# Optimization experiments

Measured on AMD Instinct MI355X. Metric: run time of the kernel, lower is better.

The kernel has to match this reference:

```python
import jax, jax.numpy as jnp
import numpy as np

# Per-level grid spatial shapes: ceil([T,H,W]/grid_size/2**i) + 1 with
# video (T,H,W) = (120,1080,1920), grid_size=8, n_levels=2.
GRID_SHAPES = [jnp.array([16.0, 136.0, 241.0], dtype=jnp.float32),
               jnp.array([9.0, 69.0, 121.0], dtype=jnp.float32)]
EMB_DIM = 16
N_PTS = 1_000_000

# 8 binary corner offsets, MSB-first bit order (matches f'{i:03b}').
OFFSETS = jnp.array([[(i >> 2) & 1, (i >> 1) & 1, i & 1] for i in range(8)],
                    dtype=jnp.float32)  # [8,3]


def setup_inputs() -> dict:
    key = jax.random.key(0)
    k0, k1, k2 = jax.random.split(key, 3)
    inputs = jax.random.uniform(k0, (N_PTS, 3), dtype=jnp.float32)
    emb0 = jax.random.normal(k1, (16, 136, 241, EMB_DIM), dtype=jnp.float32)
    emb1 = jax.random.normal(k2, (9, 69, 121, EMB_DIM), dtype=jnp.float32)
    return {"inputs": inputs, "emb0": emb0, "emb1": emb1}


def _encode_level(inputs, emb, gshape):
    # inputs: [N,3] in [0,1]; emb: [T,H,W,D]; gshape: [3] float grid shape
    coords = inputs * (gshape - 1.0)                         # [N,3]
    corner = jnp.floor(coords[:, None, :] + OFFSETS)         # [N,8,3]
    corner = jnp.clip(corner, 0.0, gshape - 1.0)             # [N,8,3]
    idx = corner.astype(jnp.int32)
    values = emb[idx[..., 0], idx[..., 1], idx[..., 2]]      # [N,8,D] gather
    weights = jnp.prod(1.0 - jnp.abs(corner - coords[:, None, :]),
                       axis=-1, keepdims=True)               # [N,8,1]
    return jnp.sum(weights * values, axis=-2)                # [N,D]


def reference(inputs, emb0, emb1):
    out0 = _encode_level(inputs, emb0, GRID_SHAPES[0])
    out1 = _encode_level(inputs, emb1, GRID_SHAPES[1])
    return jnp.concatenate([out0, out1], axis=-1)            # [N, 2*D]
```

## Files before the change

kernel.cpp:

```cpp
#include <hip/hip_runtime.h>


typedef float floatx4 __attribute__((ext_vector_type(4)));

#define KXB 8
#define KYB 17
#define KZB 31
#define NBINS (KXB * KYB * KZB)
#define NSUB 4
#define CAPS 104
#define CAP_TOT (NSUB * CAPS)
#define CNT_DWORDS (NSUB * NBINS + 1)

#define L0X 3
#define L0Y 9
#define L0Z 9
#define L0CELLS (L0X * L0Y * L0Z)
#define CSTR 20

__device__ __forceinline__ int point_key(float px, float py, float pz) {
    int ix = (int)(px * 15.0f);  ix = min(max(ix, 0), 15);
    int iy = (int)(py * 135.0f); iy = min(max(iy, 0), 135);
    int iz = (int)(pz * 240.0f); iz = min(max(iz, 0), 240);
    return ((ix >> 1) * KYB + (iy >> 3)) * KZB + (iz >> 3);
}

__device__ __forceinline__ void load4pts(const float* __restrict__ pts, int i4,
                                         float px[4], float py[4], float pz[4]) {
    const floatx4* v = (const floatx4*)(pts + (size_t)i4 * 3);
    const floatx4 a = v[0], b = v[1], c = v[2];
    px[0] = a.x; py[0] = a.y; pz[0] = a.z;
    px[1] = a.w; py[1] = b.x; pz[1] = b.y;
    px[2] = b.z; py[2] = b.w; pz[2] = c.x;
    px[3] = c.y; py[3] = c.z; pz[3] = c.w;
}

__global__ __launch_bounds__(256)
void k_zero(unsigned* __restrict__ cnt) {
    const int i = blockIdx.x * blockDim.x + threadIdx.x;
    if (i < CNT_DWORDS) cnt[i] = 0u;
}

__global__ __launch_bounds__(256)
void k_bin(const float* __restrict__ pts, int n,
           unsigned* __restrict__ cnt, unsigned* __restrict__ ovfc,
           unsigned* __restrict__ slots, unsigned* __restrict__ ovf) {
    const int i4 = (blockIdx.x * blockDim.x + threadIdx.x) * 4;
    if (i4 >= n) return;
    if (i4 + 3 < n) {
        float px[4], py[4], pz[4];
        load4pts(pts, i4, px, py, pz);
        int k[4];
#pragma unroll
        for (int j = 0; j < 4; ++j) k[j] = point_key(px[j], py[j], pz[j]);
        unsigned pos[4];
#pragma unroll
        for (int j = 0; j < 4; ++j)
            pos[j] = atomicAdd(&cnt[j * NBINS + k[j]], 1u);
#pragma unroll
        for (int j = 0; j < 4; ++j) {
            if (pos[j] < CAPS)
                slots[(size_t)k[j] * CAP_TOT + j * CAPS + pos[j]] = (unsigned)(i4 + j);
            else
                ovf[atomicAdd(ovfc, 1u)] = (unsigned)(i4 + j);
        }
    } else {
        for (int j = 0; j < 4 && i4 + j < n; ++j) {
            const size_t b = (size_t)(i4 + j) * 3;
            const int k = point_key(pts[b], pts[b+1], pts[b+2]);
            const unsigned pos = atomicAdd(&cnt[j * NBINS + k], 1u);
            if (pos < CAPS) slots[(size_t)k * CAP_TOT + j * CAPS + pos] = (unsigned)(i4 + j);
            else            ovf[atomicAdd(ovfc, 1u)] = (unsigned)(i4 + j);
        }
    }
}

__device__ __forceinline__ void setup_lds(float cx, float cy, float cz,
                                          int xb, int yb, int zb, int d,
                                          int* __restrict__ off,
                                          float* __restrict__ w) {
    float gx[2] = { floorf(cx), floorf(cx + 1.0f) };
    float gy[2] = { floorf(cy), floorf(cy + 1.0f) };
    float gz[2] = { floorf(cz), floorf(cz + 1.0f) };
    float wx[2], wy[2], wz[2];
    int   xo[2], yo[2], zo[2];
#pragma unroll
    for (int b = 0; b < 2; ++b) {
        gx[b] = fminf(fmaxf(gx[b], 0.0f), 15.0f);
        gy[b] = fminf(fmaxf(gy[b], 0.0f), 135.0f);
        gz[b] = fminf(fmaxf(gz[b], 0.0f), 240.0f);
        wx[b] = 1.0f - fabsf(gx[b] - cx);
        wy[b] = 1.0f - fabsf(gy[b] - cy);
        wz[b] = 1.0f - fabsf(gz[b] - cz);
        xo[b] = min((int)gx[b] - xb, L0X - 1) * (L0Y * L0Z * CSTR);
        yo[b] = min((int)gy[b] - yb, L0Y - 1) * (L0Z * CSTR);
        zo[b] = min((int)gz[b] - zb, L0Z - 1) * CSTR + d;
    }
    float wyz[4];
    int   yzo[4];
#pragma unroll
    for (int j = 0; j < 2; ++j)
#pragma unroll
        for (int k = 0; k < 2; ++k) {
            wyz[2 * j + k] = wy[j] * wz[k];
            yzo[2 * j + k] = yo[j] + zo[k];
        }
#pragma unroll
    for (int c = 0; c < 8; ++c) {
        const int i = (c >> 2) & 1, jk = c & 3;
        w[c]   = wx[i] * wyz[jk];
        off[c] = xo[i] + yzo[jk];
    }
}

__device__ __forceinline__ void setup_glb(float cx, float cy, float cz,
                                          float tm1, float hm1, float wm1,
                                          int sh, int sw, int d,
                                          int* __restrict__ off,
                                          float* __restrict__ w) {
    float gx[2] = { floorf(cx), floorf(cx + 1.0f) };
    float gy[2] = { floorf(cy), floorf(cy + 1.0f) };
    float gz[2] = { floorf(cz), floorf(cz + 1.0f) };
    float wx[2], wy[2], wz[2];
    int   xo[2], yo[2], zo[2];
#pragma unroll
    for (int b = 0; b < 2; ++b) {
        gx[b] = fminf(fmaxf(gx[b], 0.0f), tm1);
        gy[b] = fminf(fmaxf(gy[b], 0.0f), hm1);
        gz[b] = fminf(fmaxf(gz[b], 0.0f), wm1);
        wx[b] = 1.0f - fabsf(gx[b] - cx);
        wy[b] = 1.0f - fabsf(gy[b] - cy);
        wz[b] = 1.0f - fabsf(gz[b] - cz);
        xo[b] = (int)gx[b] * sh;
        yo[b] = (int)gy[b] * sw;
        zo[b] = (int)gz[b] * 16 + d;
    }
    float wyz[4];
    int   yzo[4];
#pragma unroll
    for (int j = 0; j < 2; ++j)
#pragma unroll
        for (int k = 0; k < 2; ++k) {
            wyz[2 * j + k] = wy[j] * wz[k];
            yzo[2 * j + k] = yo[j] + zo[k];
        }
#pragma unroll
    for (int c = 0; c < 8; ++c) {
        const int i = (c >> 2) & 1, jk = c & 3;
        w[c]   = wx[i] * wyz[jk];
        off[c] = xo[i] + yzo[jk];
    }
}

__device__ __forceinline__ void encode_glb_quad(int p, int lane4,
                                                const float* __restrict__ pts,
                                                const float* __restrict__ emb0,
                                                const float* __restrict__ emb1,
                                                float* __restrict__ out) {
    const size_t b = (size_t)p * 3;
    const float px = pts[b], py = pts[b + 1], pz = pts[b + 2];
    int   o0[8], o1[8];
    float w0[8], w1[8];
    setup_glb(px * 15.0f, py * 135.0f, pz * 240.0f, 15.0f, 135.0f, 240.0f,
              136 * 241 * 16, 241 * 16, lane4, o0, w0);
    setup_glb(px * 8.0f, py * 68.0f, pz * 120.0f, 8.0f, 68.0f, 120.0f,
              69 * 121 * 16, 121 * 16, lane4, o1, w1);
    floatx4 a0 = {0,0,0,0}, a1 = {0,0,0,0};
#pragma unroll
    for (int c = 0; c < 8; ++c) a0 += w0[c] * *(const floatx4*)(emb0 + o0[c]);
#pragma unroll
    for (int c = 0; c < 8; ++c) a1 += w1[c] * *(const floatx4*)(emb1 + o1[c]);
    float* row = out + (size_t)p * 32 + lane4;
    __builtin_nontemporal_store(a0, (floatx4*)row);
    __builtin_nontemporal_store(a1, (floatx4*)(row + 16));
}

__global__ __launch_bounds__(256, 4)
void k_main_bins(const unsigned* __restrict__ slots,
                 const unsigned* __restrict__ cnt,
                 const unsigned* __restrict__ ovfc,
                 const unsigned* __restrict__ ovf,
                 const float* __restrict__ pts,
                 const float* __restrict__ emb0,
                 const float* __restrict__ emb1,
                 float* __restrict__ out) {
    const int bin = (blockIdx.x & 7) * 527 + (blockIdx.x >> 3);
    const unsigned n0 = min(cnt[bin],             (unsigned)CAPS);
    const unsigned n1 = min(cnt[NBINS + bin],     (unsigned)CAPS);
    const unsigned n2 = min(cnt[2 * NBINS + bin], (unsigned)CAPS);
    const unsigned n3 = min(cnt[3 * NBINS + bin], (unsigned)CAPS);
    const unsigned c0 = n0, c1 = c0 + n1, c2 = c1 + n2, nt = c2 + n3;

    __shared__ float lds0[L0CELLS * CSTR];

    const int tid = threadIdx.x;
    const int d = (tid & 3) * 4;

    if (nt != 0) {
        const int bz = bin % KZB;
        const int t1 = bin / KZB;
        const int by = t1 % KYB;
        const int bx = t1 / KYB;

        const int x0 = bx * 2, y0 = by * 8, z0 = bz * 8;

        for (int idx = tid; idx < L0CELLS * 4; idx += 256) {
            const int cell = idx >> 2, q = (idx & 3) * 4;
            const int lz = cell % L0Z;
            const int t = cell / L0Z;
            const int ly = t % L0Y, lx = t / L0Y;
            const int gx = min(x0 + lx, 15), gy = min(y0 + ly, 135), gz = min(z0 + lz, 240);
            const floatx4 v = *(const floatx4*)(emb0 + ((size_t)(gx * 136 + gy) * 241 + gz) * 16 + q);
            *(floatx4*)(lds0 + cell * CSTR + q) = v;
        }
        __syncthreads();

        const int quad = tid >> 2;
        const size_t sbase = (size_t)bin * CAP_TOT;

        auto slot_of = [&](unsigned t) -> unsigned {
            const unsigned seg = (t >= c0) + (t >= c1) + (t >= c2);
            const unsigned base = (seg == 0) ? 0u : ((seg == 1) ? c0 : ((seg == 2) ? c1 : c2));
            return (unsigned)(sbase + seg * CAPS + (t - base));
        };

        unsigned tA = quad, tB = quad + 64;
        int origA = (int)slots[slot_of(min(tA, nt - 1))];
        int origB = (int)slots[slot_of(min(tB, nt - 1))];
        size_t pbA = (size_t)origA * 3;
        float pxA = pts[pbA], pyA = pts[pbA + 1], pzA = pts[pbA + 2];

        while (tA < nt) {
            const unsigned tC = tB + 64;
            const int origC = (int)slots[slot_of(min(tC, nt - 1))];
            const size_t pbB = (size_t)origB * 3;
            const float pxB = pts[pbB], pyB = pts[pbB + 1], pzB = pts[pbB + 2];

            int   o0[8], o1[8];
            float w0[8], w1[8];
            setup_lds(pxA * 15.0f, pyA * 135.0f, pzA * 240.0f, x0, y0, z0, d, o0, w0);
            setup_glb(pxA * 8.0f, pyA * 68.0f, pzA * 120.0f, 8.0f, 68.0f, 120.0f,
                      69 * 121 * 16, 121 * 16, d, o1, w1);

            floatx4 v1[8];
#pragma unroll
            for (int c = 0; c < 8; ++c) v1[c] = *(const floatx4*)(emb1 + o1[c]);
            __builtin_amdgcn_sched_barrier(0);

            floatx4 a0 = {0.f, 0.f, 0.f, 0.f}, a1 = {0.f, 0.f, 0.f, 0.f};
#pragma unroll
            for (int c = 0; c < 8; ++c) a0 += w0[c] * *(const floatx4*)(lds0 + o0[c]);
#pragma unroll
            for (int c = 0; c < 8; ++c) a1 += w1[c] * v1[c];

            float* row = out + (size_t)origA * 32 + d;
            __builtin_nontemporal_store(a0, (floatx4*)row);
            __builtin_nontemporal_store(a1, (floatx4*)(row + 16));

            tA = tB; tB = tC;
            origA = origB; origB = origC;
            pxA = pxB; pyA = pyB; pzA = pzB;
        }
    }

    if (blockIdx.x < 64) {
        const unsigned total = *ovfc;
        for (unsigned i = (blockIdx.x * 256 + tid) >> 2; i < total;
             i += (64u * 256u) >> 2) {
            encode_glb_quad((int)ovf[i], d, pts, emb0, emb1, out);
        }
    }
}

__global__ __launch_bounds__(256)
void k_main_plain(const float* __restrict__ pts,
                  const float* __restrict__ emb0,
                  const float* __restrict__ emb1,
                  float* __restrict__ out, int n) {
    const int g = blockIdx.x * blockDim.x + threadIdx.x;
    const int p = g >> 2;
    if (p >= n) return;
    encode_glb_quad(p, (g & 3) * 4, pts, emb0, emb1, out);
}

extern "C" void kernel_launch(void* const* d_in, const int* in_sizes, int n_in,
                              void* d_out, int out_size, void* d_ws, size_t ws_size,
                              hipStream_t stream) {
    const float* pts  = (const float*)d_in[0];
    const float* emb0 = (const float*)d_in[1];
    const float* emb1 = (const float*)d_in[2];
    float* out = (float*)d_out;
    const int n = in_sizes[0] / 3;

    const int block = 256;
    const int n4      = (n + 3) / 4;
    const int grid_p4 = (n4 + block - 1) / block;
    const int grid_4l = (int)(((long long)n * 4 + block - 1) / block);
    const int grid_z  = (CNT_DWORDS + block - 1) / block;

    const size_t off_cnt   = 0;
    const size_t off_ovfc  = (size_t)NSUB * NBINS * 4;
    const size_t off_slots = ((off_ovfc + 4 + 31) & ~(size_t)31);
    const size_t off_ovf   = off_slots + (size_t)NBINS * CAP_TOT * 4;
    const size_t need      = off_ovf + (size_t)n * 4;

    if (ws_size < need) {
        k_main_plain<<<grid_4l, block, 0, stream>>>(pts, emb0, emb1, out, n);
        return;
    }

    char* ws = (char*)d_ws;
    unsigned* cnt   = (unsigned*)(ws + off_cnt);
    unsigned* ovfc  = (unsigned*)(ws + off_ovfc);
    unsigned* slots = (unsigned*)(ws + off_slots);
    unsigned* ovf   = (unsigned*)(ws + off_ovf);

    k_zero<<<grid_z, block, 0, stream>>>(cnt);
    k_bin<<<grid_p4, block, 0, stream>>>(pts, n, cnt, ovfc, slots, ovf);
    k_main_bins<<<NBINS, block, 0, stream>>>(slots, cnt, ovfc, ovf,
                                             pts, emb0, emb1, out);
}
```

Measured before the change: 111.3 us.

## Store point coordinates with index in bin slots to skip indirect gather

The binning kernel now writes a 16-byte record (x, y, z, original index) into each bin slot instead of only the index. The main kernel can then read coordinates straight from the slot and no longer needs a dependent gather into the points array. Binning moves to one point per thread with the sub-bin picked by p&3, and the explicit sched_barrier is dropped, with the LDS setup moved after the level-1 loads are issued. In exchange the slot buffer grows fourfold, adding write and read traffic, and the main loop's software prefetch is cut from two points ahead to one.

Result: slower. 114.1 us (+2.5%).

```diff
diff --git a/kernel.cpp b/kernel.cpp
--- a/kernel.cpp
+++ b/kernel.cpp
@@ -25,16 +25,6 @@
     return ((ix >> 1) * KYB + (iy >> 3)) * KZB + (iz >> 3);
 }
 
-__device__ __forceinline__ void load4pts(const float* __restrict__ pts, int i4,
-                                         float px[4], float py[4], float pz[4]) {
-    const floatx4* v = (const floatx4*)(pts + (size_t)i4 * 3);
-    const floatx4 a = v[0], b = v[1], c = v[2];
-    px[0] = a.x; py[0] = a.y; pz[0] = a.z;
-    px[1] = a.w; py[1] = b.x; pz[1] = b.y;
-    px[2] = b.z; py[2] = b.w; pz[2] = c.x;
-    px[3] = c.y; py[3] = c.z; pz[3] = c.w;
-}
-
 __global__ __launch_bounds__(256)
 void k_zero(unsigned* __restrict__ cnt) {
     const int i = blockIdx.x * blockDim.x + threadIdx.x;
@@ -44,34 +34,19 @@
 __global__ __launch_bounds__(256)
 void k_bin(const float* __restrict__ pts, int n,
            unsigned* __restrict__ cnt, unsigned* __restrict__ ovfc,
-           unsigned* __restrict__ slots, unsigned* __restrict__ ovf) {
-    const int i4 = (blockIdx.x * blockDim.x + threadIdx.x) * 4;
-    if (i4 >= n) return;
-    if (i4 + 3 < n) {
-        float px[4], py[4], pz[4];
-        load4pts(pts, i4, px, py, pz);
-        int k[4];
-#pragma unroll
-        for (int j = 0; j < 4; ++j) k[j] = point_key(px[j], py[j], pz[j]);
-        unsigned pos[4];
-#pragma unroll
-        for (int j = 0; j < 4; ++j)
-            pos[j] = atomicAdd(&cnt[j * NBINS + k[j]], 1u);
-#pragma unroll
-        for (int j = 0; j < 4; ++j) {
-            if (pos[j] < CAPS)
-                slots[(size_t)k[j] * CAP_TOT + j * CAPS + pos[j]] = (unsigned)(i4 + j);
-            else
-                ovf[atomicAdd(ovfc, 1u)] = (unsigned)(i4 + j);
-        }
+           floatx4* __restrict__ slots, unsigned* __restrict__ ovf) {
+    const int p = blockIdx.x * blockDim.x + threadIdx.x;
+    if (p >= n) return;
+    const size_t b = (size_t)p * 3;
+    const float px = pts[b], py = pts[b + 1], pz = pts[b + 2];
+    const int k = point_key(px, py, pz);
+    const int sub = p & 3;
+    const unsigned pos = atomicAdd(&cnt[sub * NBINS + k], 1u);
+    if (pos < CAPS) {
+        floatx4 rec = { px, py, pz, __int_as_float(p) };
+        slots[(size_t)k * CAP_TOT + sub * CAPS + pos] = rec;
     } else {
-        for (int j = 0; j < 4 && i4 + j < n; ++j) {
-            const size_t b = (size_t)(i4 + j) * 3;
-            const int k = point_key(pts[b], pts[b+1], pts[b+2]);
-            const unsigned pos = atomicAdd(&cnt[j * NBINS + k], 1u);
-            if (pos < CAPS) slots[(size_t)k * CAP_TOT + j * CAPS + pos] = (unsigned)(i4 + j);
-            else            ovf[atomicAdd(ovfc, 1u)] = (unsigned)(i4 + j);
-        }
+        ovf[atomicAdd(ovfc, 1u)] = (unsigned)p;
     }
 }
 
@@ -176,7 +151,7 @@
 }
 
 __global__ __launch_bounds__(256, 4)
-void k_main_bins(const unsigned* __restrict__ slots,
+void k_main_bins(const floatx4* __restrict__ slots,
                  const unsigned* __restrict__ cnt,
                  const unsigned* __restrict__ ovfc,
                  const unsigned* __restrict__ ovf,
@@ -201,7 +176,6 @@
         const int t1 = bin / KZB;
         const int by = t1 % KYB;
         const int bx = t1 / KYB;
-
         const int x0 = bx * 2, y0 = by * 8, z0 = bz * 8;
 
         for (int idx = tid; idx < L0CELLS * 4; idx += 256) {
@@ -218,34 +192,28 @@
         const int quad = tid >> 2;
         const size_t sbase = (size_t)bin * CAP_TOT;
 
-        auto slot_of = [&](unsigned t) -> unsigned {
+        auto slot_of = [&](unsigned t) -> size_t {
             const unsigned seg = (t >= c0) + (t >= c1) + (t >= c2);
             const unsigned base = (seg == 0) ? 0u : ((seg == 1) ? c0 : ((seg == 2) ? c1 : c2));
-            return (unsigned)(sbase + seg * CAPS + (t - base));
+            return sbase + seg * CAPS + (t - base);
         };
 
-        unsigned tA = quad, tB = quad + 64;
-        int origA = (int)slots[slot_of(min(tA, nt - 1))];
-        int origB = (int)slots[slot_of(min(tB, nt - 1))];
-        size_t pbA = (size_t)origA * 3;
-        float pxA = pts[pbA], pyA = pts[pbA + 1], pzA = pts[pbA + 2];
-
-        while (tA < nt) {
-            const unsigned tC = tB + 64;
-            const int origC = (int)slots[slot_of(min(tC, nt - 1))];
-            const size_t pbB = (size_t)origB * 3;
-            const float pxB = pts[pbB], pyB = pts[pbB + 1], pzB = pts[pbB + 2];
+        unsigned t = quad;
+        floatx4 rec = slots[slot_of(min(t, nt - 1))];
+        while (t < nt) {
+            const floatx4 recN = slots[slot_of(min(t + 64, nt - 1))];
+
+            const float px = rec.x, py = rec.y, pz = rec.z;
+            const int orig = __float_as_int(rec.w);
 
             int   o0[8], o1[8];
             float w0[8], w1[8];
-            setup_lds(pxA * 15.0f, pyA * 135.0f, pzA * 240.0f, x0, y0, z0, d, o0, w0);
-            setup_glb(pxA * 8.0f, pyA * 68.0f, pzA * 120.0f, 8.0f, 68.0f, 120.0f,
+            setup_glb(px * 8.0f, py * 68.0f, pz * 120.0f, 8.0f, 68.0f, 120.0f,
                       69 * 121 * 16, 121 * 16, d, o1, w1);
-
             floatx4 v1[8];
 #pragma unroll
             for (int c = 0; c < 8; ++c) v1[c] = *(const floatx4*)(emb1 + o1[c]);
-            __builtin_amdgcn_sched_barrier(0);
+            setup_lds(px * 15.0f, py * 135.0f, pz * 240.0f, x0, y0, z0, d, o0, w0);
 
             floatx4 a0 = {0.f, 0.f, 0.f, 0.f}, a1 = {0.f, 0.f, 0.f, 0.f};
 #pragma unroll
@@ -253,13 +221,12 @@
 #pragma unroll
             for (int c = 0; c < 8; ++c) a1 += w1[c] * v1[c];
 
-            float* row = out + (size_t)origA * 32 + d;
+            float* row = out + (size_t)orig * 32 + d;
             __builtin_nontemporal_store(a0, (floatx4*)row);
             __builtin_nontemporal_store(a1, (floatx4*)(row + 16));
 
-            tA = tB; tB = tC;
-            origA = origB; origB = origC;
-            pxA = pxB; pyA = pyB; pzA = pzB;
+            rec = recN;
+            t += 64;
         }
     }
 
@@ -293,15 +260,14 @@
     const int n = in_sizes[0] / 3;
 
     const int block = 256;
-    const int n4      = (n + 3) / 4;
-    const int grid_p4 = (n4 + block - 1) / block;
+    const int grid_pt = (n + block - 1) / block;
     const int grid_4l = (int)(((long long)n * 4 + block - 1) / block);
     const int grid_z  = (CNT_DWORDS + block - 1) / block;
 
     const size_t off_cnt   = 0;
     const size_t off_ovfc  = (size_t)NSUB * NBINS * 4;
-    const size_t off_slots = ((off_ovfc + 4 + 31) & ~(size_t)31);
-    const size_t off_ovf   = off_slots + (size_t)NBINS * CAP_TOT * 4;
+    const size_t off_slots = ((off_ovfc + 4 + 15) & ~(size_t)15);
+    const size_t off_ovf   = off_slots + (size_t)NBINS * CAP_TOT * 16;
     const size_t need      = off_ovf + (size_t)n * 4;
 
     if (ws_size < need) {
@@ -312,11 +278,11 @@
     char* ws = (char*)d_ws;
     unsigned* cnt   = (unsigned*)(ws + off_cnt);
     unsigned* ovfc  = (unsigned*)(ws + off_ovfc);
-    unsigned* slots = (unsigned*)(ws + off_slots);
+    floatx4*  slots = (floatx4*)(ws + off_slots);
     unsigned* ovf   = (unsigned*)(ws + off_ovf);
 
     k_zero<<<grid_z, block, 0, stream>>>(cnt);
-    k_bin<<<grid_p4, block, 0, stream>>>(pts, n, cnt, ovfc, slots, ovf);
+    k_bin<<<grid_pt, block, 0, stream>>>(pts, n, cnt, ovfc, slots, ovf);
     k_main_bins<<<NBINS, block, 0, stream>>>(slots, cnt, ovfc, ovf,
                                              pts, emb0, emb1, out);
 }
```
